# Optimization experiments

Measured on AMD Instinct MI355X. Metric: run time of the kernel, lower is better.

The kernel has to match this reference:

```python
import jax, jax.numpy as jnp
import numpy as np


def setup_inputs() -> dict:
    key = jax.random.key(0)
    kK, kV, kQ = jax.random.split(key, 3)
    B, D, S = 4, 64, 4096
    K = jax.random.normal(kK, (B, D, S), dtype=jnp.float32)
    V = jax.random.normal(kV, (B, D, S), dtype=jnp.float32)
    Q = jax.random.normal(kQ, (B, D, S), dtype=jnp.float32)
    return {"K": K, "V": V, "Q": Q}


def reference(K, V, Q):
    # K,V: [B, D, Sk], Q: [B, D, Sq]
    d = Q.shape[1]
    # A[b,k,q] = sum_d K[b,d,k] * Q[b,d,q] / sqrt(d)
    A = jnp.einsum("bdk,bdq->bkq", K, Q) / jnp.sqrt(jnp.asarray(d, Q.dtype))
    A = jax.nn.softmax(A, axis=1)  # normalize over keys (dim 1), matching F.softmax(A, 1)
    # R[b,d,q] = sum_k V[b,d,k] * A[b,k,q]
    R = jnp.einsum("bdk,bkq->bdq", V, A)
    return jnp.concatenate((R, Q), axis=1)  # [B, 2D, Sq]
```

## Files before the change

kernel.cpp:

```cpp
#include <hip/hip_runtime.h>
#include <hip/hip_bf16.h>

#define S_LEN 4096
#define D_DIM 64
#define QB 256
#define KB 32
#define NT (S_LEN / KB)
#define TILE_E 4096

typedef __attribute__((ext_vector_type(8)))  short bf16x8;
typedef __attribute__((ext_vector_type(16))) float f32x16;
typedef unsigned int u32;

#define Z16 {0.f,0.f,0.f,0.f,0.f,0.f,0.f,0.f,0.f,0.f,0.f,0.f,0.f,0.f,0.f,0.f}

union bpack8 { __hip_bfloat16 h[8]; bf16x8 v; };
union ppack  { u32 w[4]; bf16x8 v; };
union bload4 { uint2 u; __hip_bfloat16 h[4]; };

static __device__ __forceinline__ float fexp2(float x) {
    return __builtin_amdgcn_exp2f(x);
}
static __device__ __forceinline__ u32 cvtpk(float lo, float hi) {
    u32 r;
    asm("v_cvt_pk_bf16_f32 %0, %1, %2" : "=v"(r) : "v"(lo), "v"(hi));
    return r;
}
static __device__ __forceinline__ void plswap(u32 &a, u32 &b) {
    asm("v_permlane32_swap_b32 %0, %1" : "+v"(a), "+v"(b));
}

struct pfrag { ppack p0, p1; };
static __device__ __forceinline__ pfrag packP(const f32x16& s) {
    u32 A = cvtpk(s[0],  s[1]),  Bw = cvtpk(s[2],  s[3]);
    u32 C = cvtpk(s[4],  s[5]),  Dw = cvtpk(s[6],  s[7]);
    u32 E = cvtpk(s[8],  s[9]),  F  = cvtpk(s[10], s[11]);
    u32 G = cvtpk(s[12], s[13]), H  = cvtpk(s[14], s[15]);
    plswap(A, C); plswap(Bw, Dw); plswap(E, G); plswap(F, H);
    pfrag r;
    r.p0.w[0] = A; r.p0.w[1] = Bw; r.p0.w[2] = C; r.p0.w[3] = Dw;
    r.p1.w[0] = E; r.p1.w[1] = F;  r.p1.w[2] = G; r.p1.w[3] = H;
    return r;
}
static __device__ __forceinline__ float treesum(const f32x16& s) {
    float a0 = (s[0] + s[1])   + (s[2] + s[3]);
    float a1 = (s[4] + s[5])   + (s[6] + s[7]);
    float a2 = (s[8] + s[9])   + (s[10] + s[11]);
    float a3 = (s[12] + s[13]) + (s[14] + s[15]);
    return (a0 + a1) + (a2 + a3);
}

#define GLD16(gp, lp) __builtin_amdgcn_global_load_lds( \
    (const __attribute__((address_space(1))) u32*)(const void*)(gp), \
    (__attribute__((address_space(3))) u32*)(void*)(lp), 16, 0, 0)

#define QSCALE 0.18033688011112042f

__global__ __launch_bounds__(256)
void prep_all(const float* __restrict__ K, const float* __restrict__ V,
              const float* __restrict__ Q,
              __hip_bfloat16* __restrict__ KVbf, __hip_bfloat16* __restrict__ Qbf,
              float* __restrict__ out)
{
    const int b = blockIdx.y, x = blockIdx.x, z = blockIdx.z;
    const int t = threadIdx.x;

    if (z == 0) {
        const int key = t & 31, dg = t >> 5;
        const float* src = K + ((size_t)b * D_DIM + dg * 8) * S_LEN + x * KB + key;
        bpack8 u;
        #pragma unroll
        for (int e = 0; e < 8; ++e)
            u.h[e] = __float2bfloat16(src[(size_t)e * S_LEN]);
        *(bf16x8*)&KVbf[((size_t)b * NT + x) * TILE_E + t * 8] = u.v;
    } else if (z == 1) {
        const int kg = t >> 6, d = t & 63;
        const float* p = V + ((size_t)b * D_DIM + d) * S_LEN + x * KB + kg * 8;
        float4 a = *(const float4*)p, c = *(const float4*)(p + 4);
        bpack8 u;
        u.h[0] = __float2bfloat16(a.x); u.h[1] = __float2bfloat16(a.y);
        u.h[2] = __float2bfloat16(a.z); u.h[3] = __float2bfloat16(a.w);
        u.h[4] = __float2bfloat16(c.x); u.h[5] = __float2bfloat16(c.y);
        u.h[6] = __float2bfloat16(c.z); u.h[7] = __float2bfloat16(c.w);
        *(bf16x8*)&KVbf[((size_t)b * NT + x) * TILE_E + 2048 + t * 8] = u.v;
    } else {
        const int q = x * 32 + (t & 31), dg = t >> 5;
        const float* src = Q + ((size_t)b * D_DIM + dg * 8) * S_LEN + q;
        float r[8];
        #pragma unroll
        for (int e = 0; e < 8; ++e) r[e] = src[(size_t)e * S_LEN];
        float* o = out + ((size_t)b * 2 * D_DIM + D_DIM + dg * 8) * S_LEN + q;
        #pragma unroll
        for (int e = 0; e < 8; ++e) o[(size_t)e * S_LEN] = r[e];
        bpack8 u;
        #pragma unroll
        for (int e = 0; e < 8; ++e) u.h[e] = __float2bfloat16(r[e] * QSCALE);
        *(bf16x8*)&Qbf[((size_t)b * S_LEN + q) * D_DIM + dg * 8] = u.v;
    }
}

__global__ __launch_bounds__(256, 2)
void attn_fwd(const __hip_bfloat16* __restrict__ KVbf,
              const __hip_bfloat16* __restrict__ Qbf,
              float* __restrict__ out,
              __hip_bfloat16* __restrict__ accPb, float* __restrict__ lP,
              int ntiles, int nb, int direct)
{
    const int b  = blockIdx.y;
    const int z  = blockIdx.z;
    const int q0 = blockIdx.x * QB;

    const int t    = threadIdx.x;
    const int lane = t & 63;
    const int w    = t >> 6;
    const int l5   = lane & 31;
    const int h    = lane >> 5;

    __shared__ __align__(16) char Ls[2][16384];

    const __hip_bfloat16* kvb = KVbf + ((size_t)b * NT + (size_t)z * ntiles) * TILE_E;

    const __hip_bfloat16* qrowA = Qbf + ((size_t)b * S_LEN + q0 + w * 64 + l5) * D_DIM;
    const __hip_bfloat16* qrowB = qrowA + 32 * D_DIM;
    bf16x8 qfA[4], qfB[4];
    #pragma unroll
    for (int j = 0; j < 4; ++j) {
        qfA[j] = *(const bf16x8*)&qrowA[(2 * j + h) * 8];
        qfB[j] = *(const bf16x8*)&qrowB[(2 * j + h) * 8];
    }

    #pragma unroll
    for (int sub = 0; sub < 2; ++sub) {
        GLD16(kvb + sub * TILE_E + t * 8,        Ls[0] + sub * 8192 + w * 1024);
        GLD16(kvb + sub * TILE_E + 2048 + t * 8, Ls[0] + sub * 8192 + 4096 + w * 1024);
    }
    __syncthreads();

    float lsumA = 0.f, lsumB = 0.f;
    f32x16 accA[2] = {Z16, Z16}, accB[2] = {Z16, Z16};
    int cur = 0;

    const int npairs = ntiles >> 1;
    for (int p = 0; p < npairs; ++p) {
        if (p + 1 < npairs) {
            const __hip_bfloat16* nx = kvb + (size_t)(2 * p + 2) * TILE_E;
            #pragma unroll
            for (int sub = 0; sub < 2; ++sub) {
                GLD16(nx + sub * TILE_E + t * 8,
                      Ls[cur ^ 1] + sub * 8192 + w * 1024);
                GLD16(nx + sub * TILE_E + 2048 + t * 8,
                      Ls[cur ^ 1] + sub * 8192 + 4096 + w * 1024);
            }
        }

        #pragma unroll
        for (int sub = 0; sub < 2; ++sub) {
            const char* Lk = Ls[cur] + sub * 8192;
            const char* Lv = Lk + 4096;

            bf16x8 kf[4];
            #pragma unroll
            for (int j = 0; j < 4; ++j)
                kf[j] = *(const bf16x8*)(Lk + ((2 * j + h) * 32 + l5) * 16);

            f32x16 sA = Z16, sB = Z16;
            __builtin_amdgcn_s_setprio(1);
            #pragma unroll
            for (int j = 0; j < 4; ++j) {
                sA = __builtin_amdgcn_mfma_f32_32x32x16_bf16(kf[j], qfA[j], sA, 0, 0, 0);
                sB = __builtin_amdgcn_mfma_f32_32x32x16_bf16(kf[j], qfB[j], sB, 0, 0, 0);
            }
            __builtin_amdgcn_s_setprio(0);

            bf16x8 vf[4];
            #pragma unroll
            for (int j = 0; j < 2; ++j)
                #pragma unroll
                for (int dt = 0; dt < 2; ++dt)
                    vf[2 * j + dt] = *(const bf16x8*)(Lv + ((2 * j + h) * 64 + dt * 32 + l5) * 16);

            #pragma unroll
            for (int r = 0; r < 16; ++r) sA[r] = fexp2(sA[r]);
            #pragma unroll
            for (int r = 0; r < 16; ++r) sB[r] = fexp2(sB[r]);
            lsumA += treesum(sA);
            lsumB += treesum(sB);

            pfrag pA = packP(sA), pB = packP(sB);

            __builtin_amdgcn_s_setprio(1);
            #pragma unroll
            for (int j = 0; j < 2; ++j)
                #pragma unroll
                for (int dt = 0; dt < 2; ++dt) {
                    const bf16x8 vv = vf[2 * j + dt];
                    const ppack& pa = j ? pA.p1 : pA.p0;
                    const ppack& pb = j ? pB.p1 : pB.p0;
                    accA[dt] = __builtin_amdgcn_mfma_f32_32x32x16_bf16(vv, pa.v, accA[dt], 0, 0, 0);
                    accB[dt] = __builtin_amdgcn_mfma_f32_32x32x16_bf16(vv, pb.v, accB[dt], 0, 0, 0);
                }
            __builtin_amdgcn_s_setprio(0);
        }

        __syncthreads();
        cur ^= 1;
    }

    lsumA += __shfl_xor(lsumA, 32);
    lsumB += __shfl_xor(lsumB, 32);

    const int qA = q0 + w * 64 + l5;
    if (!direct) {
        __hip_bfloat16* ap = accPb + (size_t)(z * nb + b) * D_DIM * S_LEN;
        #pragma unroll
        for (int dt = 0; dt < 2; ++dt)
            #pragma unroll
            for (int r = 0; r < 16; ++r) {
                int d = dt * 32 + (r & 3) + 8 * (r >> 2) + 4 * h;
                ap[(size_t)d * S_LEN + qA]      = __float2bfloat16(accA[dt][r]);
                ap[(size_t)d * S_LEN + qA + 32] = __float2bfloat16(accB[dt][r]);
            }
        if (h == 0) {
            lP[(size_t)(z * nb + b) * S_LEN + qA]      = lsumA;
            lP[(size_t)(z * nb + b) * S_LEN + qA + 32] = lsumB;
        }
    } else {
        float invA = 1.f / lsumA, invB = 1.f / lsumB;
        float* op = out + (size_t)b * 2 * D_DIM * S_LEN;
        #pragma unroll
        for (int dt = 0; dt < 2; ++dt)
            #pragma unroll
            for (int r = 0; r < 16; ++r) {
                int d = dt * 32 + (r & 3) + 8 * (r >> 2) + 4 * h;
                op[(size_t)d * S_LEN + qA]      = accA[dt][r] * invA;
                op[(size_t)d * S_LEN + qA + 32] = accB[dt][r] * invB;
            }
    }
}

__global__ __launch_bounds__(256)
void attn_combine(const __hip_bfloat16* __restrict__ accPb,
                  const float* __restrict__ lP,
                  float* __restrict__ out, int nsplit, int nb)
{
    int gid = blockIdx.x * 256 + threadIdx.x;
    int q4   = gid & (S_LEN / 4 - 1);
    int rest = gid >> 10;
    int d    = rest & (D_DIM - 1);
    int b    = rest >> 6;
    if (b >= nb) return;
    size_t qoff = (size_t)q4 * 4;

    float num[4] = {0.f,0.f,0.f,0.f}, den[4] = {0.f,0.f,0.f,0.f};
    for (int z = 0; z < nsplit; ++z) {
        bload4 a;
        a.u = *(const uint2*)&accPb[((size_t)(z * nb + b) * D_DIM + d) * S_LEN + qoff];
        float4 lz = *(const float4*)&lP[(size_t)(z * nb + b) * S_LEN + qoff];
        num[0] += __bfloat162float(a.h[0]); num[1] += __bfloat162float(a.h[1]);
        num[2] += __bfloat162float(a.h[2]); num[3] += __bfloat162float(a.h[3]);
        den[0] += lz.x; den[1] += lz.y; den[2] += lz.z; den[3] += lz.w;
    }
    float4 r;
    r.x = num[0] / den[0]; r.y = num[1] / den[1];
    r.z = num[2] / den[2]; r.w = num[3] / den[3];
    *(float4*)&out[((size_t)b * 2 * D_DIM + d) * S_LEN + qoff] = r;
}

extern "C" void kernel_launch(void* const* d_in, const int* in_sizes, int n_in,
                              void* d_out, int out_size, void* d_ws, size_t ws_size,
                              hipStream_t stream) {
    const float* K = (const float*)d_in[0];
    const float* V = (const float*)d_in[1];
    const float* Q = (const float*)d_in[2];
    float* out = (float*)d_out;

    const int B = in_sizes[0] / (D_DIM * S_LEN);
    const size_t kvE = (size_t)B * NT * TILE_E;
    const size_t qE  = (size_t)B * S_LEN * D_DIM;

    auto need = [&](int ns) -> size_t {
        return (kvE + qE) * 2
             + (size_t)ns * B * D_DIM * S_LEN * 2
             + (size_t)ns * B * S_LEN * 4;
    };
    const int cand[4] = {8, 4, 2, 1};
    int nsplit = 1;
    for (int i = 0; i < 4; ++i)
        if (need(cand[i]) <= ws_size) { nsplit = cand[i]; break; }
    const int direct = (nsplit == 1);

    __hip_bfloat16* KVbf = (__hip_bfloat16*)d_ws;
    __hip_bfloat16* Qbf  = KVbf + kvE;
    __hip_bfloat16* accPb = Qbf + qE;
    float* lP = (float*)(accPb + (size_t)nsplit * B * D_DIM * S_LEN);

    prep_all<<<dim3(NT, B, 3), dim3(256), 0, stream>>>(K, V, Q, KVbf, Qbf, out);

    attn_fwd<<<dim3(S_LEN / QB, B, nsplit), dim3(256), 0, stream>>>(
        KVbf, Qbf, out, accPb, lP, NT / nsplit, B, direct);

    if (!direct) {
        int total = B * D_DIM * (S_LEN / 4);
        attn_combine<<<dim3(total / 256), dim3(256), 0, stream>>>(
            accPb, lP, out, nsplit, B);
    }
}
```

Before: 38.31 us.

## Split keys across waves in-block and reduce partials in LDS, drop combine kernel

Instead of splitting the key range across grid z and merging bf16 partials through global memory in a separate combine kernel, each 512-thread block now handles 64 queries and each of its 8 waves covers one eighth of the keys. Each wave double-buffers its own key/value tiles in a private LDS region, so the per-tile block barriers become per-wave vmcnt waits. Partial sums and accumulators are then reduced through LDS and written directly as normalized fp32. This removes the partial round trip through global memory and one launch, at the cost of 128KB of LDS per block, which limits blocks per CU.

```diff
diff --git a/kernel.cpp b/kernel.cpp
--- a/kernel.cpp
+++ b/kernel.cpp
@@ -3,7 +3,7 @@
 
 #define S_LEN 4096
 #define D_DIM 64
-#define QB 256
+#define QB 64
 #define KB 32
 #define NT (S_LEN / KB)
 #define TILE_E 4096
@@ -16,7 +16,6 @@
 
 union bpack8 { __hip_bfloat16 h[8]; bf16x8 v; };
 union ppack  { u32 w[4]; bf16x8 v; };
-union bload4 { uint2 u; __hip_bfloat16 h[4]; };
 
 static __device__ __forceinline__ float fexp2(float x) {
     return __builtin_amdgcn_exp2f(x);
@@ -99,28 +98,26 @@
     }
 }
 
-__global__ __launch_bounds__(256, 2)
+__global__ __launch_bounds__(512, 2)
 void attn_fwd(const __hip_bfloat16* __restrict__ KVbf,
               const __hip_bfloat16* __restrict__ Qbf,
-              float* __restrict__ out,
-              __hip_bfloat16* __restrict__ accPb, float* __restrict__ lP,
-              int ntiles, int nb, int direct)
+              float* __restrict__ out)
 {
     const int b  = blockIdx.y;
-    const int z  = blockIdx.z;
     const int q0 = blockIdx.x * QB;
-
-    const int t    = threadIdx.x;
+    const int t  = threadIdx.x;
     const int lane = t & 63;
     const int w    = t >> 6;
     const int l5   = lane & 31;
     const int h    = lane >> 5;
 
-    __shared__ __align__(16) char Ls[2][16384];
-
-    const __hip_bfloat16* kvb = KVbf + ((size_t)b * NT + (size_t)z * ntiles) * TILE_E;
-
-    const __hip_bfloat16* qrowA = Qbf + ((size_t)b * S_LEN + q0 + w * 64 + l5) * D_DIM;
+    __shared__ __align__(16) char Ls[131072];
+    char* myL = Ls + w * 16384;
+
+    const int WT = NT / 8;
+    const __hip_bfloat16* kvb = KVbf + ((size_t)b * NT + w * WT) * TILE_E;
+
+    const __hip_bfloat16* qrowA = Qbf + ((size_t)b * S_LEN + q0 + l5) * D_DIM;
     const __hip_bfloat16* qrowB = qrowA + 32 * D_DIM;
     bf16x8 qfA[4], qfB[4];
     #pragma unroll
@@ -130,140 +127,113 @@
     }
 
     #pragma unroll
-    for (int sub = 0; sub < 2; ++sub) {
-        GLD16(kvb + sub * TILE_E + t * 8,        Ls[0] + sub * 8192 + w * 1024);
-        GLD16(kvb + sub * TILE_E + 2048 + t * 8, Ls[0] + sub * 8192 + 4096 + w * 1024);
-    }
-    __syncthreads();
+    for (int i = 0; i < 8; ++i)
+        GLD16(kvb + i * 512 + lane * 8, myL + i * 1024);
+    asm volatile("s_waitcnt vmcnt(0)" ::: "memory");
+    __builtin_amdgcn_sched_barrier(0);
 
     float lsumA = 0.f, lsumB = 0.f;
     f32x16 accA[2] = {Z16, Z16}, accB[2] = {Z16, Z16};
     int cur = 0;
 
-    const int npairs = ntiles >> 1;
-    for (int p = 0; p < npairs; ++p) {
-        if (p + 1 < npairs) {
-            const __hip_bfloat16* nx = kvb + (size_t)(2 * p + 2) * TILE_E;
+    for (int it = 0; it < WT; ++it) {
+        if (it + 1 < WT) {
+            const __hip_bfloat16* nx = kvb + (size_t)(it + 1) * TILE_E;
             #pragma unroll
-            for (int sub = 0; sub < 2; ++sub) {
-                GLD16(nx + sub * TILE_E + t * 8,
-                      Ls[cur ^ 1] + sub * 8192 + w * 1024);
-                GLD16(nx + sub * TILE_E + 2048 + t * 8,
-                      Ls[cur ^ 1] + sub * 8192 + 4096 + w * 1024);
+            for (int i = 0; i < 8; ++i)
+                GLD16(nx + i * 512 + lane * 8, myL + (cur ^ 1) * 8192 + i * 1024);
+        }
+        const char* Lk = myL + cur * 8192;
+        const char* Lv = Lk + 4096;
+
+        bf16x8 kf[4];
+        #pragma unroll
+        for (int j = 0; j < 4; ++j)
+            kf[j] = *(const bf16x8*)(Lk + ((2 * j + h) * 32 + l5) * 16);
+
+        f32x16 sA = Z16, sB = Z16;
+        __builtin_amdgcn_s_setprio(1);
+        #pragma unroll
+        for (int j = 0; j < 4; ++j) {
+            sA = __builtin_amdgcn_mfma_f32_32x32x16_bf16(kf[j], qfA[j], sA, 0, 0, 0);
+            sB = __builtin_amdgcn_mfma_f32_32x32x16_bf16(kf[j], qfB[j], sB, 0, 0, 0);
+        }
+        __builtin_amdgcn_s_setprio(0);
+
+        bf16x8 vf[4];
+        #pragma unroll
+        for (int j = 0; j < 2; ++j)
+            #pragma unroll
+            for (int dt = 0; dt < 2; ++dt)
+                vf[2 * j + dt] = *(const bf16x8*)(Lv + ((2 * j + h) * 64 + dt * 32 + l5) * 16);
+
+        #pragma unroll
+        for (int r = 0; r < 16; ++r) sA[r] = fexp2(sA[r]);
+        #pragma unroll
+        for (int r = 0; r < 16; ++r) sB[r] = fexp2(sB[r]);
+        lsumA += treesum(sA);
+        lsumB += treesum(sB);
+
+        pfrag pA = packP(sA), pB = packP(sB);
+
+        __builtin_amdgcn_s_setprio(1);
+        #pragma unroll
+        for (int j = 0; j < 2; ++j)
+            #pragma unroll
+            for (int dt = 0; dt < 2; ++dt) {
+                const bf16x8 vv = vf[2 * j + dt];
+                const ppack& pa = j ? pA.p1 : pA.p0;
+                const ppack& pb = j ? pB.p1 : pB.p0;
+                accA[dt] = __builtin_amdgcn_mfma_f32_32x32x16_bf16(vv, pa.v, accA[dt], 0, 0, 0);
+                accB[dt] = __builtin_amdgcn_mfma_f32_32x32x16_bf16(vv, pb.v, accB[dt], 0, 0, 0);
             }
-        }
-
-        #pragma unroll
-        for (int sub = 0; sub < 2; ++sub) {
-            const char* Lk = Ls[cur] + sub * 8192;
-            const char* Lv = Lk + 4096;
-
-            bf16x8 kf[4];
-            #pragma unroll
-            for (int j = 0; j < 4; ++j)
-                kf[j] = *(const bf16x8*)(Lk + ((2 * j + h) * 32 + l5) * 16);
-
-            f32x16 sA = Z16, sB = Z16;
-            __builtin_amdgcn_s_setprio(1);
-            #pragma unroll
-            for (int j = 0; j < 4; ++j) {
-                sA = __builtin_amdgcn_mfma_f32_32x32x16_bf16(kf[j], qfA[j], sA, 0, 0, 0);
-                sB = __builtin_amdgcn_mfma_f32_32x32x16_bf16(kf[j], qfB[j], sB, 0, 0, 0);
-            }
-            __builtin_amdgcn_s_setprio(0);
-
-            bf16x8 vf[4];
-            #pragma unroll
-            for (int j = 0; j < 2; ++j)
-                #pragma unroll
-                for (int dt = 0; dt < 2; ++dt)
-                    vf[2 * j + dt] = *(const bf16x8*)(Lv + ((2 * j + h) * 64 + dt * 32 + l5) * 16);
-
-            #pragma unroll
-            for (int r = 0; r < 16; ++r) sA[r] = fexp2(sA[r]);
-            #pragma unroll
-            for (int r = 0; r < 16; ++r) sB[r] = fexp2(sB[r]);
-            lsumA += treesum(sA);
-            lsumB += treesum(sB);
-
-            pfrag pA = packP(sA), pB = packP(sB);
-
-            __builtin_amdgcn_s_setprio(1);
-            #pragma unroll
-            for (int j = 0; j < 2; ++j)
-                #pragma unroll
-                for (int dt = 0; dt < 2; ++dt) {
-                    const bf16x8 vv = vf[2 * j + dt];
-                    const ppack& pa = j ? pA.p1 : pA.p0;
-                    const ppack& pb = j ? pB.p1 : pB.p0;
-                    accA[dt] = __builtin_amdgcn_mfma_f32_32x32x16_bf16(vv, pa.v, accA[dt], 0, 0, 0);
-                    accB[dt] = __builtin_amdgcn_mfma_f32_32x32x16_bf16(vv, pb.v, accB[dt], 0, 0, 0);
-                }
-            __builtin_amdgcn_s_setprio(0);
-        }
-
-        __syncthreads();
+        __builtin_amdgcn_s_setprio(0);
+
+        asm volatile("s_waitcnt vmcnt(0)" ::: "memory");
+        __builtin_amdgcn_sched_barrier(0);
         cur ^= 1;
     }
 
     lsumA += __shfl_xor(lsumA, 32);
     lsumB += __shfl_xor(lsumB, 32);
 
-    const int qA = q0 + w * 64 + l5;
-    if (!direct) {
-        __hip_bfloat16* ap = accPb + (size_t)(z * nb + b) * D_DIM * S_LEN;
-        #pragma unroll
-        for (int dt = 0; dt < 2; ++dt)
-            #pragma unroll
-            for (int r = 0; r < 16; ++r) {
-                int d = dt * 32 + (r & 3) + 8 * (r >> 2) + 4 * h;
-                ap[(size_t)d * S_LEN + qA]      = __float2bfloat16(accA[dt][r]);
-                ap[(size_t)d * S_LEN + qA + 32] = __float2bfloat16(accB[dt][r]);
-            }
-        if (h == 0) {
-            lP[(size_t)(z * nb + b) * S_LEN + qA]      = lsumA;
-            lP[(size_t)(z * nb + b) * S_LEN + qA + 32] = lsumB;
+    float* LF = (float*)Ls;
+    __syncthreads();
+    if (h == 0) {
+        LF[w * 64 + l5]      = lsumA;
+        LF[w * 64 + 32 + l5] = lsumB;
+    }
+    __syncthreads();
+    const int qp = t & 63;
+    float den = 0.f;
+    #pragma unroll
+    for (int w2 = 0; w2 < 8; ++w2) den += LF[w2 * 64 + qp];
+    const float inv = 1.f / den;
+    __syncthreads();
+
+    #pragma unroll
+    for (int dt = 0; dt < 2; ++dt)
+        #pragma unroll
+        for (int r = 0; r < 16; ++r) {
+            int d = dt * 32 + (r & 3) + 8 * (r >> 2) + 4 * h;
+            LF[w * 2048 + d * 32 + l5]         = accA[dt][r];
+            LF[16384 + w * 2048 + d * 32 + l5] = accB[dt][r];
         }
-    } else {
-        float invA = 1.f / lsumA, invB = 1.f / lsumB;
-        float* op = out + (size_t)b * 2 * D_DIM * S_LEN;
-        #pragma unroll
-        for (int dt = 0; dt < 2; ++dt)
-            #pragma unroll
-            for (int r = 0; r < 16; ++r) {
-                int d = dt * 32 + (r & 3) + 8 * (r >> 2) + 4 * h;
-                op[(size_t)d * S_LEN + qA]      = accA[dt][r] * invA;
-                op[(size_t)d * S_LEN + qA + 32] = accB[dt][r] * invB;
-            }
-    }
-}
-
-__global__ __launch_bounds__(256)
-void attn_combine(const __hip_bfloat16* __restrict__ accPb,
-                  const float* __restrict__ lP,
-                  float* __restrict__ out, int nsplit, int nb)
-{
-    int gid = blockIdx.x * 256 + threadIdx.x;
-    int q4   = gid & (S_LEN / 4 - 1);
-    int rest = gid >> 10;
-    int d    = rest & (D_DIM - 1);
-    int b    = rest >> 6;
-    if (b >= nb) return;
-    size_t qoff = (size_t)q4 * 4;
-
-    float num[4] = {0.f,0.f,0.f,0.f}, den[4] = {0.f,0.f,0.f,0.f};
-    for (int z = 0; z < nsplit; ++z) {
-        bload4 a;
-        a.u = *(const uint2*)&accPb[((size_t)(z * nb + b) * D_DIM + d) * S_LEN + qoff];
-        float4 lz = *(const float4*)&lP[(size_t)(z * nb + b) * S_LEN + qoff];
-        num[0] += __bfloat162float(a.h[0]); num[1] += __bfloat162float(a.h[1]);
-        num[2] += __bfloat162float(a.h[2]); num[3] += __bfloat162float(a.h[3]);
-        den[0] += lz.x; den[1] += lz.y; den[2] += lz.z; den[3] += lz.w;
-    }
-    float4 r;
-    r.x = num[0] / den[0]; r.y = num[1] / den[1];
-    r.z = num[2] / den[2]; r.w = num[3] / den[3];
-    *(float4*)&out[((size_t)b * 2 * D_DIM + d) * S_LEN + qoff] = r;
+    __syncthreads();
+
+    const int dgrp = t >> 6;
+    const int slab = (qp < 32) ? 0 : 16384;
+    const int qs   = qp & 31;
+    float* op = out + (size_t)b * 2 * D_DIM * S_LEN + q0 + qp;
+    #pragma unroll
+    for (int dd = 0; dd < 8; ++dd) {
+        int d = dgrp * 8 + dd;
+        float sum = 0.f;
+        #pragma unroll
+        for (int w2 = 0; w2 < 8; ++w2)
+            sum += LF[slab + w2 * 2048 + d * 32 + qs];
+        op[(size_t)d * S_LEN] = sum * inv;
+    }
 }
 
 extern "C" void kernel_launch(void* const* d_in, const int* in_sizes, int n_in,
@@ -276,32 +246,11 @@
 
     const int B = in_sizes[0] / (D_DIM * S_LEN);
     const size_t kvE = (size_t)B * NT * TILE_E;
-    const size_t qE  = (size_t)B * S_LEN * D_DIM;
-
-    auto need = [&](int ns) -> size_t {
-        return (kvE + qE) * 2
-             + (size_t)ns * B * D_DIM * S_LEN * 2
-             + (size_t)ns * B * S_LEN * 4;
-    };
-    const int cand[4] = {8, 4, 2, 1};
-    int nsplit = 1;
-    for (int i = 0; i < 4; ++i)
-        if (need(cand[i]) <= ws_size) { nsplit = cand[i]; break; }
-    const int direct = (nsplit == 1);
 
     __hip_bfloat16* KVbf = (__hip_bfloat16*)d_ws;
     __hip_bfloat16* Qbf  = KVbf + kvE;
-    __hip_bfloat16* accPb = Qbf + qE;
-    float* lP = (float*)(accPb + (size_t)nsplit * B * D_DIM * S_LEN);
 
     prep_all<<<dim3(NT, B, 3), dim3(256), 0, stream>>>(K, V, Q, KVbf, Qbf, out);
 
-    attn_fwd<<<dim3(S_LEN / QB, B, nsplit), dim3(256), 0, stream>>>(
-        KVbf, Qbf, out, accPb, lP, NT / nsplit, B, direct);
-
-    if (!direct) {
-        int total = B * D_DIM * (S_LEN / 4);
-        attn_combine<<<dim3(total / 256), dim3(256), 0, stream>>>(
-            accPb, lP, out, nsplit, B);
-    }
-}
+    attn_fwd<<<dim3(S_LEN / QB, B), dim3(512), 0, stream>>>(KVbf, Qbf, out);
+}
```

Result: faster. 35.56 us (-7.2%).
